# Kernel tuning notes

Measured on AMD Instinct MI355X. Metric: run time of the kernel, lower is better.

The kernel has to match this reference:

```python
import jax, jax.numpy as jnp
import numpy as np

D_MODEL = 1024
NUM_HEADS = 16


def setup_inputs() -> dict:
    key = jax.random.key(0)
    ks = jax.random.split(key, 11)
    B, L, D = 1, 4096, D_MODEL
    s = 1.0 / np.sqrt(D)
    inp = {
        "Q": jax.random.normal(ks[0], (B, L, D), jnp.float32),
        "K": jax.random.normal(ks[1], (B, L, D), jnp.float32),
        "V": jax.random.normal(ks[2], (B, L, D), jnp.float32),
        "w_q": jax.random.normal(ks[3], (D, D), jnp.float32) * s,
        "b_q": jax.random.normal(ks[4], (D,), jnp.float32) * s,
        "w_k": jax.random.normal(ks[5], (D, D), jnp.float32) * s,
        "b_k": jax.random.normal(ks[6], (D,), jnp.float32) * s,
        "w_v": jax.random.normal(ks[7], (D, D), jnp.float32) * s,
        "b_v": jax.random.normal(ks[8], (D,), jnp.float32) * s,
        "w_o": jax.random.normal(ks[9], (D, D), jnp.float32) * s,
        "b_o": jax.random.normal(ks[10], (D,), jnp.float32) * s,
    }
    return inp


def _split_heads(x, n_heads):
    B, L, D = x.shape
    return x.reshape(B, L, n_heads, D // n_heads).transpose(0, 2, 1, 3)  # (B,H,L,Dh)


def reference(Q, K, V, w_q, b_q, w_k, b_k, w_v, b_v, w_o, b_o):
    H = NUM_HEADS
    # QKV projections (torch Linear: x @ W.T + b)
    q = _split_heads(Q @ w_q.T + b_q, H)
    k = _split_heads(K @ w_k.T + b_k, H)
    v = _split_heads(V @ w_v.T + b_v, H)
    d_h = q.shape[-1]
    scores = jnp.einsum("bhqd,bhkd->bhqk", q, k) / jnp.sqrt(jnp.float32(d_h))
    attn = jax.nn.softmax(scores, axis=-1)
    out = jnp.einsum("bhqk,bhkd->bhqd", attn, v)  # (B,H,L,Dh)
    B, _, L, _ = out.shape
    out = out.transpose(0, 2, 1, 3).reshape(B, L, H * d_h)
    return out @ w_o.T + b_o
```

## Files before the change

kernel.cpp:

```cpp
#include <hip/hip_runtime.h>
#include <hip/hip_bf16.h>
#include <stdint.h>

#define D_MODEL 1024
#define NHEAD   16
#define DH      64

typedef __attribute__((ext_vector_type(8))) short bf16x8;
typedef __attribute__((ext_vector_type(4))) float f32x4;

__device__ __forceinline__ ushort f2bf(float f) {
    __hip_bfloat16 h = __float2bfloat16(f);
    return *reinterpret_cast<ushort*>(&h);
}

__device__ __forceinline__ void gload_lds16(const void* g, void* l) {
    __builtin_amdgcn_global_load_lds(
        (const __attribute__((address_space(1))) void*)g,
        (__attribute__((address_space(3))) void*)l, 16, 0, 0);
}

__device__ __forceinline__ bf16x8 load8f(const float* p) {
    const float4 a = *(const float4*)p;
    const float4 b = *(const float4*)(p + 4);
    bf16x8 r;
    r[0] = (short)f2bf(a.x); r[1] = (short)f2bf(a.y);
    r[2] = (short)f2bf(a.z); r[3] = (short)f2bf(a.w);
    r[4] = (short)f2bf(b.x); r[5] = (short)f2bf(b.y);
    r[6] = (short)f2bf(b.z); r[7] = (short)f2bf(b.w);
    return r;
}

__global__ __launch_bounds__(256) void cvt_w_kernel(
    const float* __restrict__ w0, const float* __restrict__ w1,
    const float* __restrict__ w2, const float* __restrict__ w3,
    ushort* __restrict__ out)
{
    const int g = blockIdx.x * 256 + threadIdx.x;
    const int m = g >> 17;
    const int off = (g & 131071) * 8;
    const float* src = (m == 0) ? w0 : (m == 1) ? w1 : (m == 2) ? w2 : w3;
    *(bf16x8*)(out + (size_t)m * 1048576 + off) = load8f(src + off);
}

__global__ __launch_bounds__(256) void cvt_all_kernel(
    const float* __restrict__ w0, const float* __restrict__ w1,
    const float* __restrict__ w2, const float* __restrict__ w3,
    const float* __restrict__ X0, const float* __restrict__ X1,
    const float* __restrict__ X2,
    ushort* __restrict__ Wb,
    ushort* __restrict__ Qb, ushort* __restrict__ Kb, ushort* __restrict__ Vb,
    int igrp)
{
    const int g = blockIdx.x * 256 + threadIdx.x;
    if (g < 524288) {
        const int m = g >> 17;
        const int off = (g & 131071) * 8;
        const float* src = (m == 0) ? w0 : (m == 1) ? w1 : (m == 2) ? w2 : w3;
        *(bf16x8*)(Wb + (size_t)m * 1048576 + off) = load8f(src + off);
    } else {
        const int g2 = g - 524288;
        if (g2 >= 3 * igrp) return;
        const int m = g2 / igrp;
        const int off = (g2 - m * igrp) * 8;
        const float* src = (m == 0) ? X0 : (m == 1) ? X1 : X2;
        ushort* dst = (m == 0) ? Qb : (m == 1) ? Kb : Vb;
        *(bf16x8*)(dst + off) = load8f(src + off);
    }
}

__device__ __forceinline__ void storeC(float*  C, size_t i, float v) { C[i] = v; }
__device__ __forceinline__ void storeC(ushort* C, size_t i, float v) { C[i] = (short)f2bf(v); }

__device__ __forceinline__ void xcd_swizzle(int& bx, int& by) {
    if (gridDim.x == 8 && (gridDim.y & 7) == 0) {
        const int fid   = by * 8 + bx;
        const int xcd   = fid & 7;
        const int local = fid >> 3;
        const int rpx   = gridDim.y >> 3;
        by = xcd * rpx + (local >> 3);
        bx = local & 7;
    }
}

template<int NW, bool A_F32, typename TX, typename TOUT>
__device__ __forceinline__ void gemm_core(
    const TX* __restrict__ X,
    const ushort* __restrict__ Wb,
    const float* __restrict__ Bias,
    TOUT* __restrict__ C,
    int M, int N, int K, float scale,
    int bx, int by,
    short* As, short* Bs)
{
    const int tid  = threadIdx.x;
    const int w    = tid >> 6;
    const int lane = tid & 63;
    const int quad = lane >> 4;
    const int l15  = lane & 15;
    const int wr   = (NW == 4) ? (w >> 1) : (w >> 2);
    const int wc   = (NW == 4) ? (w & 1)  : (w & 3);
    const int NJ   = (NW == 4) ? 4 : 2;
    const int colw = (NW == 4) ? 64 : 32;

    const int m0 = by * 128;
    const int n0 = bx * 128;

    f32x4 acc[4][4] = {};

    for (int k0 = 0; k0 < K; k0 += 32) {
        __syncthreads();
        #pragma unroll
        for (int c = 0; c < 8 / NW; ++c) {
            int chunk = w * (8 / NW) + c;
            int row   = chunk * 16 + (lane >> 2);
            gload_lds16(Wb + (size_t)(n0 + row) * K + k0 + (lane & 3) * 8,
                        &Bs[chunk * 512]);
        }
        if constexpr (A_F32) {
            #pragma unroll
            for (int c = 0; c < 2; ++c) {
                int idx = c * 256 + tid;
                int row = idx >> 2;
                int col = (idx & 3) * 8;
                *(bf16x8*)&As[row * 32 + col] =
                    load8f((const float*)X + (size_t)(m0 + row) * K + k0 + col);
            }
        } else {
            #pragma unroll
            for (int c = 0; c < 8 / NW; ++c) {
                int chunk = w * (8 / NW) + c;
                int row   = chunk * 16 + (lane >> 2);
                gload_lds16((const ushort*)X + (size_t)(m0 + row) * K + k0 + (lane & 3) * 8,
                            &As[chunk * 512]);
            }
        }
        __syncthreads();

        bf16x8 af[4], bfr[4];
        #pragma unroll
        for (int i = 0; i < 4; ++i)
            af[i] = *(const bf16x8*)&As[(wr * 64 + i * 16 + l15) * 32 + quad * 8];
        #pragma unroll
        for (int j = 0; j < NJ; ++j)
            bfr[j] = *(const bf16x8*)&Bs[(wc * colw + j * 16 + l15) * 32 + quad * 8];
        #pragma unroll
        for (int i = 0; i < 4; ++i)
            #pragma unroll
            for (int j = 0; j < NJ; ++j)
                acc[i][j] = __builtin_amdgcn_mfma_f32_16x16x32_bf16(af[i], bfr[j], acc[i][j], 0, 0, 0);
    }

    float bias[4];
    #pragma unroll
    for (int j = 0; j < NJ; ++j)
        bias[j] = Bias[n0 + wc * colw + j * 16 + l15];

    #pragma unroll
    for (int i = 0; i < 4; ++i) {
        int row = m0 + wr * 64 + i * 16 + quad * 4;
        #pragma unroll
        for (int j = 0; j < NJ; ++j) {
            int col = n0 + wc * colw + j * 16 + l15;
            #pragma unroll
            for (int r = 0; r < 4; ++r)
                storeC(C, (size_t)(row + r) * N + col, (acc[i][j][r] + bias[j]) * scale);
        }
    }
}

__global__ __launch_bounds__(256) void qkv_proj_f32_kernel(
    const float* __restrict__ Qin, const float* __restrict__ Kin,
    const float* __restrict__ Vin,
    const ushort* __restrict__ Wb,
    const float* __restrict__ Bq, const float* __restrict__ Bk,
    const float* __restrict__ Bv,
    ushort* qo, ushort* ko, ushort* vo, int L)
{
    __shared__ short As[4096];
    __shared__ short Bs[4096];
    const int z = blockIdx.z;
    const float *X, *B; ushort* C;
    float scale = 1.0f;
    if (z == 0)      { X = Qin; B = Bq; C = qo; scale = 0.125f * 1.44269504088896f; }
    else if (z == 1) { X = Kin; B = Bk; C = ko; }
    else             { X = Vin; B = Bv; C = vo; }
    int bx = blockIdx.x, by = blockIdx.y;
    xcd_swizzle(bx, by);
    gemm_core<4, true, float, ushort>(X, Wb + (size_t)z * 1048576, B, C,
                                      L, D_MODEL, D_MODEL, scale, bx, by, As, Bs);
}

__global__ __launch_bounds__(256) void qkv_proj_bf16_kernel(
    const ushort* __restrict__ Qb, const ushort* __restrict__ Kb,
    const ushort* __restrict__ Vb,
    const ushort* __restrict__ Wb,
    const float* __restrict__ Bq, const float* __restrict__ Bk,
    const float* __restrict__ Bv,
    ushort* qo, ushort* ko, ushort* vo, int L)
{
    __shared__ short As[4096];
    __shared__ short Bs[4096];

    const int gy    = gridDim.y;
    const int slice = gy * 8;
    const int total = slice * 3;
    const int phys  = (blockIdx.z * gy + blockIdx.y) * 8 + blockIdx.x;
    int lz, lx, ly;
    if ((total & 7) == 0) {
        const int logical = (phys & 7) * (total >> 3) + (phys >> 3);
        lz = logical / slice;
        const int lrem = logical - lz * slice;
        ly = lrem >> 3;
        lx = lrem & 7;
    } else {
        lz = blockIdx.z; ly = blockIdx.y; lx = blockIdx.x;
    }

    const ushort *X; const float* B; ushort* C;
    float scale = 1.0f;
    if (lz == 0)      { X = Qb; B = Bq; C = qo; scale = 0.125f * 1.44269504088896f; }
    else if (lz == 1) { X = Kb; B = Bk; C = ko; }
    else              { X = Vb; B = Bv; C = vo; }
    gemm_core<4, false, ushort, ushort>(X, Wb + (size_t)lz * 1048576, B, C,
                                        L, D_MODEL, D_MODEL, scale, lx, ly, As, Bs);
}

__global__ __launch_bounds__(512) void out_proj_kernel(
    const ushort* __restrict__ Xa, const ushort* __restrict__ Wb,
    const float* __restrict__ Bo, float* out, int L)
{
    __shared__ short As[4096];
    __shared__ short Bs[4096];
    int bx = blockIdx.x, by = blockIdx.y;
    xcd_swizzle(bx, by);
    gemm_core<8, false, ushort, float>(Xa, Wb + (size_t)3 * 1048576, Bo, out,
                                       L, D_MODEL, D_MODEL, 1.0f, bx, by, As, Bs);
}

__global__ __launch_bounds__(512) void attn_kernel(
    const ushort* __restrict__ Qw,
    const ushort* __restrict__ Kw,
    const ushort* __restrict__ Vw,
    ushort* __restrict__ Ow, int L)
{
    __shared__ short Ks[64 * 64];
    __shared__ short Vs[64 * 64];
    __shared__ short Ps[8][16 * 64];

    const int tid  = threadIdx.x;
    const int w    = tid >> 6;
    const int lane = tid & 63;
    const int quad = lane >> 4;
    const int l15  = lane & 15;

    const int p   = blockIdx.y * gridDim.x + blockIdx.x;
    const int slot = p >> 3;
    const int h   = (p & 7) * 2 + (slot >> 5);
    const int q0  = (slot & 31) * 128;

    const ushort* qp = Qw + (size_t)(q0 + w * 16 + l15) * D_MODEL + h * DH + quad * 8;
    bf16x8 qf0 = *(const bf16x8*)(qp);
    bf16x8 qf1 = *(const bf16x8*)(qp + 32);

    const int kkey = tid >> 3;
    const int kc8  = tid & 7;
    const int vkey = lane;
    const int vdh  = w * 8;

    const int krswz0 = ((quad    ) ^ (l15 & 7)) * 8;
    const int krswz1 = ((quad + 4) ^ (l15 & 7)) * 8;

    const int kwofs = kkey * 64 + ((kc8 ^ (kkey & 7)) * 8);

    f32x4 o[4] = {};
    float l_run = 0.f;

    const size_t dstep = (size_t)64 * D_MODEL;
    const ushort* kp = Kw + (size_t)kkey * D_MODEL + h * DH + kc8 * 8;
    const ushort* vp = Vw + (size_t)vkey * D_MODEL + h * DH + vdh;

    bf16x8 k0 = *(const bf16x8*)kp;
    bf16x8 v0 = *(const bf16x8*)vp;
    bf16x8 k1 = *(const bf16x8*)(kp + dstep);
    bf16x8 v1 = *(const bf16x8*)(vp + dstep);

    const int NT = L >> 6;

    auto compute = [&]() {
        f32x4 st[4];
        __builtin_amdgcn_s_setprio(1);
        #pragma unroll
        for (int kt = 0; kt < 4; ++kt) {
            const int kr = (kt * 16 + l15) * 64;
            bf16x8 kf0 = *(const bf16x8*)&Ks[kr + krswz0];
            bf16x8 kf1 = *(const bf16x8*)&Ks[kr + krswz1];
            f32x4 z = {};
            z = __builtin_amdgcn_mfma_f32_16x16x32_bf16(kf0, qf0, z, 0, 0, 0);
            z = __builtin_amdgcn_mfma_f32_16x16x32_bf16(kf1, qf1, z, 0, 0, 0);
            st[kt] = z;
        }
        __builtin_amdgcn_s_setprio(0);

        float rs = 0.f;
        #pragma unroll
        for (int kt = 0; kt < 4; ++kt) {
            float p0 = __builtin_amdgcn_exp2f(st[kt][0]);
            float p1 = __builtin_amdgcn_exp2f(st[kt][1]);
            float p2 = __builtin_amdgcn_exp2f(st[kt][2]);
            float p3 = __builtin_amdgcn_exp2f(st[kt][3]);
            rs += (p0 + p1) + (p2 + p3);
            uint2 pk;
            pk.x = (uint32_t)f2bf(p0) | ((uint32_t)f2bf(p1) << 16);
            pk.y = (uint32_t)f2bf(p2) | ((uint32_t)f2bf(p3) << 16);
            const int G = kt * 2 + (quad >> 1);
            *(uint2*)&Ps[w][l15 * 64 + ((G ^ (l15 & 7)) * 8) + (quad & 1) * 4] = pk;
        }
        l_run += rs;

        __builtin_amdgcn_s_setprio(1);
        #pragma unroll
        for (int f = 0; f < 2; ++f) {
            bf16x8 pf = *(const bf16x8*)&Ps[w][l15 * 64 + (((f * 4 + quad) ^ (l15 & 7)) * 8)];
            #pragma unroll
            for (int dt = 0; dt < 4; ++dt) {
                bf16x8 vf = *(const bf16x8*)&Vs[(dt * 16 + l15) * 64 + (((f * 4 + quad) ^ (l15 & 7)) * 8)];
                o[dt] = __builtin_amdgcn_mfma_f32_16x16x32_bf16(pf, vf, o[dt], 0, 0, 0);
            }
        }
        __builtin_amdgcn_s_setprio(0);
    };

    for (int t = 0; t < NT; t += 2) {
        __syncthreads();
        *(bf16x8*)&Ks[kwofs] = k0;
        #pragma unroll
        for (int i = 0; i < 8; ++i)
            Vs[(vdh + i) * 64 + (((vkey >> 3) ^ i) * 8) + (vkey & 7)] = v0[i];
        __syncthreads();
        if (t + 2 < NT) {
            kp += 2 * dstep;
            vp += 2 * dstep;
            k0 = *(const bf16x8*)kp;
            v0 = *(const bf16x8*)vp;
        }
        compute();

        __syncthreads();
        *(bf16x8*)&Ks[kwofs] = k1;
        #pragma unroll
        for (int i = 0; i < 8; ++i)
            Vs[(vdh + i) * 64 + (((vkey >> 3) ^ i) * 8) + (vkey & 7)] = v1[i];
        __syncthreads();
        if (t + 3 < NT) {
            k1 = *(const bf16x8*)(kp + dstep);
            v1 = *(const bf16x8*)(vp + dstep);
        }
        compute();
    }

    l_run += __shfl_xor(l_run, 16);
    l_run += __shfl_xor(l_run, 32);
    const float inv = 1.f / l_run;
    #pragma unroll
    for (int r = 0; r < 4; ++r) {
        const float linv = __shfl(inv, (lane & 48) | (quad * 4 + r));
        const int row = q0 + w * 16 + quad * 4 + r;
        #pragma unroll
        for (int dt = 0; dt < 4; ++dt) {
            int col = h * DH + dt * 16 + l15;
            Ow[(size_t)row * D_MODEL + col] = (short)f2bf(o[dt][r] * linv);
        }
    }
}

extern "C" void kernel_launch(void* const* d_in, const int* in_sizes, int n_in,
                              void* d_out, int out_size, void* d_ws, size_t ws_size,
                              hipStream_t stream) {
    const float* Q   = (const float*)d_in[0];
    const float* K   = (const float*)d_in[1];
    const float* V   = (const float*)d_in[2];
    const float* w_q = (const float*)d_in[3];
    const float* b_q = (const float*)d_in[4];
    const float* w_k = (const float*)d_in[5];
    const float* b_k = (const float*)d_in[6];
    const float* w_v = (const float*)d_in[7];
    const float* b_v = (const float*)d_in[8];
    const float* w_o = (const float*)d_in[9];
    const float* b_o = (const float*)d_in[10];
    float* out = (float*)d_out;

    const int L = in_sizes[0] / D_MODEL;
    const size_t mat = (size_t)L * D_MODEL;

    ushort* Wb   = (ushort*)d_ws;
    ushort* q_ws = (ushort*)d_out;
    ushort* k_ws = q_ws + mat;
    const bool ext = ws_size >= (size_t)40 * 1024 * 1024;

    ushort *a_ws, *v_ws, *Qb = nullptr, *Kb = nullptr, *Vb = nullptr;
    if (ext) {
        Vb   = (ushort*)d_ws + 4 * 1048576;
        v_ws = Vb + mat;
        Qb   = v_ws + mat;
        Kb   = Qb + mat;
        a_ws = Vb;
    } else {
        a_ws = (ushort*)d_ws + 4 * 1048576;
        v_ws = a_ws + mat;
    }

    if (ext) {
        const int igrp = (int)(mat / 8);
        const int total = 524288 + 3 * igrp;
        cvt_all_kernel<<<dim3((total + 255) / 256), dim3(256), 0, stream>>>(
            w_q, w_k, w_v, w_o, Q, K, V, Wb, Qb, Kb, Vb, igrp);
        dim3 gqkv(D_MODEL / 128, L / 128, 3);
        qkv_proj_bf16_kernel<<<gqkv, dim3(256), 0, stream>>>(Qb, Kb, Vb, Wb,
                                                             b_q, b_k, b_v,
                                                             q_ws, k_ws, v_ws, L);
    } else {
        cvt_w_kernel<<<dim3(2048), dim3(256), 0, stream>>>(w_q, w_k, w_v, w_o, Wb);
        dim3 gqkv(D_MODEL / 128, L / 128, 3);
        qkv_proj_f32_kernel<<<gqkv, dim3(256), 0, stream>>>(Q, K, V, Wb,
                                                            b_q, b_k, b_v,
                                                            q_ws, k_ws, v_ws, L);
    }
    dim3 gattn(L / 128, NHEAD);
    attn_kernel<<<gattn, dim3(512), 0, stream>>>(q_ws, k_ws, v_ws, a_ws, L);
    dim3 gout(D_MODEL / 128, L / 128);
    out_proj_kernel<<<gout, dim3(512), 0, stream>>>(a_ws, Wb, b_o, out, L);
}
```

Before: 263.9 us.

## Double attention query tile to 256 rows with split K/V staging roles

The attention kernel now runs 1024-thread blocks covering 256 query rows per head, so each K/V tile staged in LDS is shared by twice as many queries. Global K/V loads are divided by role: the first 512 threads load K and the rest load V, which halves the per-thread staging registers. The grid drops to 256 blocks, fewer than before, and 1024-thread blocks may lower occupancy and raise the cost of each barrier.

```diff
diff --git a/kernel.cpp b/kernel.cpp
--- a/kernel.cpp
+++ b/kernel.cpp
@@ -238,7 +238,7 @@
                                        L, D_MODEL, D_MODEL, 1.0f, bx, by, As, Bs);
 }
 
-__global__ __launch_bounds__(512) void attn_kernel(
+__global__ __launch_bounds__(1024) void attn_kernel(
     const ushort* __restrict__ Qw,
     const ushort* __restrict__ Kw,
     const ushort* __restrict__ Vw,
@@ -246,7 +246,7 @@
 {
     __shared__ short Ks[64 * 64];
     __shared__ short Vs[64 * 64];
-    __shared__ short Ps[8][16 * 64];
+    __shared__ short Ps[16][16 * 64];
 
     const int tid  = threadIdx.x;
     const int w    = tid >> 6;
@@ -254,19 +254,21 @@
     const int quad = lane >> 4;
     const int l15  = lane & 15;
 
-    const int p   = blockIdx.y * gridDim.x + blockIdx.x;
+    const int p    = blockIdx.y * gridDim.x + blockIdx.x;
     const int slot = p >> 3;
-    const int h   = (p & 7) * 2 + (slot >> 5);
-    const int q0  = (slot & 31) * 128;
+    const int h    = (p & 7) * 2 + (slot >> 4);
+    const int q0   = (slot & 15) * 256;
 
     const ushort* qp = Qw + (size_t)(q0 + w * 16 + l15) * D_MODEL + h * DH + quad * 8;
     bf16x8 qf0 = *(const bf16x8*)(qp);
     bf16x8 qf1 = *(const bf16x8*)(qp + 32);
 
+    const bool krole = (tid < 512);
     const int kkey = tid >> 3;
     const int kc8  = tid & 7;
-    const int vkey = lane;
-    const int vdh  = w * 8;
+    const int vt   = tid & 511;
+    const int vkey = vt & 63;
+    const int vdh  = (vt >> 6) * 8;
 
     const int krswz0 = ((quad    ) ^ (l15 & 7)) * 8;
     const int krswz1 = ((quad + 4) ^ (l15 & 7)) * 8;
@@ -277,15 +279,24 @@
     float l_run = 0.f;
 
     const size_t dstep = (size_t)64 * D_MODEL;
-    const ushort* kp = Kw + (size_t)kkey * D_MODEL + h * DH + kc8 * 8;
-    const ushort* vp = Vw + (size_t)vkey * D_MODEL + h * DH + vdh;
-
-    bf16x8 k0 = *(const bf16x8*)kp;
-    bf16x8 v0 = *(const bf16x8*)vp;
-    bf16x8 k1 = *(const bf16x8*)(kp + dstep);
-    bf16x8 v1 = *(const bf16x8*)(vp + dstep);
+    const ushort* sp = krole
+        ? (Kw + (size_t)kkey * D_MODEL + h * DH + kc8 * 8)
+        : (Vw + (size_t)vkey * D_MODEL + h * DH + vdh);
+
+    bf16x8 r0 = *(const bf16x8*)sp;
+    bf16x8 r1 = *(const bf16x8*)(sp + dstep);
 
     const int NT = L >> 6;
+
+    auto stage = [&](const bf16x8& rg) {
+        if (krole) {
+            *(bf16x8*)&Ks[kwofs] = rg;
+        } else {
+            #pragma unroll
+            for (int i = 0; i < 8; ++i)
+                Vs[(vdh + i) * 64 + (((vkey >> 3) ^ i) * 8) + (vkey & 7)] = rg[i];
+        }
+    };
 
     auto compute = [&]() {
         f32x4 st[4];
@@ -333,28 +344,19 @@
 
     for (int t = 0; t < NT; t += 2) {
         __syncthreads();
-        *(bf16x8*)&Ks[kwofs] = k0;
-        #pragma unroll
-        for (int i = 0; i < 8; ++i)
-            Vs[(vdh + i) * 64 + (((vkey >> 3) ^ i) * 8) + (vkey & 7)] = v0[i];
+        stage(r0);
         __syncthreads();
         if (t + 2 < NT) {
-            kp += 2 * dstep;
-            vp += 2 * dstep;
-            k0 = *(const bf16x8*)kp;
-            v0 = *(const bf16x8*)vp;
+            sp += 2 * dstep;
+            r0 = *(const bf16x8*)sp;
         }
         compute();
 
         __syncthreads();
-        *(bf16x8*)&Ks[kwofs] = k1;
-        #pragma unroll
-        for (int i = 0; i < 8; ++i)
-            Vs[(vdh + i) * 64 + (((vkey >> 3) ^ i) * 8) + (vkey & 7)] = v1[i];
+        stage(r1);
         __syncthreads();
         if (t + 3 < NT) {
-            k1 = *(const bf16x8*)(kp + dstep);
-            v1 = *(const bf16x8*)(vp + dstep);
+            r1 = *(const bf16x8*)(sp + dstep);
         }
         compute();
     }
@@ -426,8 +428,8 @@
                                                             b_q, b_k, b_v,
                                                             q_ws, k_ws, v_ws, L);
     }
-    dim3 gattn(L / 128, NHEAD);
-    attn_kernel<<<gattn, dim3(512), 0, stream>>>(q_ws, k_ws, v_ws, a_ws, L);
+    dim3 gattn(L / 256, NHEAD);
+    attn_kernel<<<gattn, dim3(1024), 0, stream>>>(q_ws, k_ws, v_ws, a_ws, L);
     dim3 gout(D_MODEL / 128, L / 128);
     out_proj_kernel<<<gout, dim3(512), 0, stream>>>(a_ws, Wb, b_o, out, L);
 }
```

Result: faster. 256.4 us (median of 2 runs) (-2.8%).
